# Kernel optimization log

Measured on AMD Instinct MI355X. Metric: run time of the kernel, lower is better.

## Reference

```python
import jax, jax.numpy as jnp
import numpy as np

B, LQ, LK = 4, 2048, 2048
DQ, DK, DO = 1024, 1024, 1024


def setup_inputs() -> dict:
    key = jax.random.key(0)
    ks = jax.random.split(key, 9)
    s = 0.02
    return {
        "query_input": jax.random.normal(ks[0], (B, LQ, DQ), jnp.float32),
        "key_input": jax.random.normal(ks[1], (B, LK, DK), jnp.float32),
        "value_input": jax.random.normal(ks[2], (B, LK, DK), jnp.float32),
        "Wq": jax.random.normal(ks[3], (DQ, DO), jnp.float32) * s,
        "bq": jax.random.normal(ks[4], (DO,), jnp.float32) * s,
        "Wk": jax.random.normal(ks[5], (DK, DO), jnp.float32) * s,
        "bk": jax.random.normal(ks[6], (DO,), jnp.float32) * s,
        "Wv": jax.random.normal(ks[7], (DK, DO), jnp.float32) * s,
        "bv": jax.random.normal(ks[8], (DO,), jnp.float32) * s,
    }


def reference(query_input, key_input, value_input, Wq, bq, Wk, bk, Wv, bv):
    scale = jnp.asarray(DO, query_input.dtype) ** 0.5
    q = query_input @ Wq + bq              # [B, Lq, D]
    k = key_input @ Wk + bk                # [B, Lk, D]
    v = value_input @ Wv + bv              # [B, Lk, D]
    attn = jnp.einsum("bqd,bkd->bqk", q, k) / scale
    attn = jax.nn.softmax(attn, axis=-1)
    return jnp.einsum("bqk,bkd->bqd", attn, v)
```

## Files before the change

kernel.cpp:

```cpp
#include <hip/hip_runtime.h>

typedef _Float16 f16x8 __attribute__((ext_vector_type(8)));
typedef _Float16 f16x4 __attribute__((ext_vector_type(4)));
typedef float f32x4 __attribute__((ext_vector_type(4)));

__device__ __forceinline__ void lds_load16(const _Float16* g, _Float16* l) {
    __builtin_amdgcn_global_load_lds(
        (const __attribute__((address_space(1))) void*)g,
        (__attribute__((address_space(3))) void*)l,
        16, 0, 0);
}

template <int BIAS_MODE, bool OUT_F32>
__global__ __launch_bounds__(256, 2)
void gemm_nt_f16(const _Float16* __restrict__ A, const _Float16* __restrict__ B,
                 void* __restrict__ Cv, const float* __restrict__ bias,
                 int M, int N, int K, int lda, int ldb, int ldc,
                 long long strideA, long long strideB, long long strideC,
                 float alpha)
{
    const int z = blockIdx.z;
    A += (size_t)z * strideA;
    B += (size_t)z * strideB;

    const int m0 = blockIdx.y * 128;
    const int n0 = blockIdx.x * 128;

    __shared__ __align__(16) _Float16 As[128 * 32];
    __shared__ __align__(16) _Float16 Bs[128 * 32];

    const int t    = threadIdx.x;
    const int w    = t >> 6;
    const int lane = t & 63;
    const int ln   = lane & 15;
    const int kq   = lane >> 4;
    const int wm   = (w & 1) * 64;
    const int wn   = (w >> 1) * 64;

    const int arow = t >> 2;
    const int kc   = (t & 3) * 8;
    const _Float16* gA0 = A + (size_t)(m0 + arow) * lda + kc;
    const _Float16* gA1 = A + (size_t)(m0 + 64 + arow) * lda + kc;
    const _Float16* gB0 = B + (size_t)(n0 + arow) * ldb + kc;
    const _Float16* gB1 = B + (size_t)(n0 + 64 + arow) * ldb + kc;
    _Float16* lA0 = As + w * 512;
    _Float16* lA1 = As + 2048 + w * 512;
    _Float16* lB0 = Bs + w * 512;
    _Float16* lB1 = Bs + 2048 + w * 512;

    f32x4 acc[4][4] = {};

    for (int k0 = 0; k0 < K; k0 += 32) {
        __syncthreads();
        lds_load16(gA0 + k0, lA0);
        lds_load16(gA1 + k0, lA1);
        lds_load16(gB0 + k0, lB0);
        lds_load16(gB1 + k0, lB1);
        __syncthreads();

        f16x8 af[4], bf[4];
#pragma unroll
        for (int i = 0; i < 4; ++i)
            af[i] = *(const f16x8*)(As + (wm + i * 16 + ln) * 32 + kq * 8);
#pragma unroll
        for (int i = 0; i < 4; ++i)
            bf[i] = *(const f16x8*)(Bs + (wn + i * 16 + ln) * 32 + kq * 8);
#pragma unroll
        for (int i = 0; i < 4; ++i)
#pragma unroll
            for (int j = 0; j < 4; ++j)
                acc[i][j] = __builtin_amdgcn_mfma_f32_16x16x32_f16(af[i], bf[j], acc[i][j], 0, 0, 0);
    }

    float*     Cf = (float*)Cv;
    _Float16*  Ch = (_Float16*)Cv;
    const size_t cbase = (size_t)z * strideC;
#pragma unroll
    for (int i = 0; i < 4; ++i) {
        const int rbase = m0 + wm + i * 16 + kq * 4;
#pragma unroll
        for (int j = 0; j < 4; ++j) {
            const int gcol = n0 + wn + j * 16 + ln;
#pragma unroll
            for (int r = 0; r < 4; ++r) {
                float vv = acc[i][j][r] * alpha;
                if (BIAS_MODE == 1) vv += bias[gcol];
                if (BIAS_MODE == 2) vv += bias[rbase + r];
                const size_t idx = cbase + (size_t)(rbase + r) * ldc + gcol;
                if (OUT_F32) Cf[idx] = vv;
                else         Ch[idx] = (_Float16)vv;
            }
        }
    }
}

__global__ __launch_bounds__(256)
void cvt_f32_f16(const float4* __restrict__ x, _Float16* __restrict__ y)
{
    const size_t i = (size_t)blockIdx.x * 256 + threadIdx.x;
    float4 f = x[i];
    f16x4 o = { (_Float16)f.x, (_Float16)f.y, (_Float16)f.z, (_Float16)f.w };
    *(f16x4*)(y + i * 4) = o;
}

__global__ __launch_bounds__(256)
void transpose_w_1024(const float* __restrict__ W, _Float16* __restrict__ WT)
{
    __shared__ float tile[32][33];
    const int bx = blockIdx.x * 32;
    const int by = blockIdx.y * 32;
    const int tx = threadIdx.x;
    const int ty = threadIdx.y;
#pragma unroll
    for (int i = ty; i < 32; i += 8)
        tile[i][tx] = W[(size_t)(by + i) * 1024 + bx + tx];
    __syncthreads();
#pragma unroll
    for (int i = ty; i < 32; i += 8)
        WT[(size_t)(bx + i) * 1024 + by + tx] = (_Float16)tile[tx][i];
}

__global__ __launch_bounds__(256)
void softmax_rows_2048(_Float16* __restrict__ S)
{
    const size_t row = blockIdx.x;
    _Float16* p = S + row * 2048;
    const int t = threadIdx.x, lane = t & 63, w = t >> 6;

    f16x8 v = *(const f16x8*)(p + t * 8);
    float x[8];
    float mx = -3.4e38f;
#pragma unroll
    for (int i = 0; i < 8; ++i) { x[i] = (float)v[i]; mx = fmaxf(mx, x[i]); }
#pragma unroll
    for (int off = 32; off > 0; off >>= 1) mx = fmaxf(mx, __shfl_xor(mx, off));

    __shared__ float rmax[4], rsum[4];
    if (lane == 0) rmax[w] = mx;
    __syncthreads();
    mx = fmaxf(fmaxf(rmax[0], rmax[1]), fmaxf(rmax[2], rmax[3]));

    float s = 0.f;
#pragma unroll
    for (int i = 0; i < 8; ++i) { x[i] = __expf(x[i] - mx); s += x[i]; }
#pragma unroll
    for (int off = 32; off > 0; off >>= 1) s += __shfl_xor(s, off);
    if (lane == 0) rsum[w] = s;
    __syncthreads();
    s = rsum[0] + rsum[1] + rsum[2] + rsum[3];

    const float inv = 1.f / s;
    f16x8 o;
#pragma unroll
    for (int i = 0; i < 8; ++i) o[i] = (_Float16)(x[i] * inv);
    *(f16x8*)(p + t * 8) = o;
}

extern "C" void kernel_launch(void* const* d_in, const int* in_sizes, int n_in,
                              void* d_out, int out_size, void* d_ws, size_t ws_size,
                              hipStream_t stream)
{
    const float* Xq = (const float*)d_in[0];
    const float* Xk = (const float*)d_in[1];
    const float* Xv = (const float*)d_in[2];
    const float* Wq = (const float*)d_in[3];
    const float* bq = (const float*)d_in[4];
    const float* Wk = (const float*)d_in[5];
    const float* bk = (const float*)d_in[6];
    const float* Wv = (const float*)d_in[7];
    const float* bv = (const float*)d_in[8];
    float* out = (float*)d_out;

    const size_t XN = (size_t)8192 * 1024;
    const size_t WN = (size_t)1024 * 1024;

    _Float16* ws  = (_Float16*)d_ws;
    _Float16* Xqh = ws;
    _Float16* Xkh = Xqh + XN;
    _Float16* Xvh = Xkh + XN;
    _Float16* WqT = Xvh + XN;
    _Float16* WkT = WqT + WN;
    _Float16* WvT = WkT + WN;
    _Float16* qh  = WvT + WN;
    _Float16* kh  = qh + XN;
    _Float16* vT  = kh + XN;
    _Float16* S   = vT + XN;

    cvt_f32_f16<<<8192, 256, 0, stream>>>((const float4*)Xq, Xqh);
    cvt_f32_f16<<<8192, 256, 0, stream>>>((const float4*)Xk, Xkh);
    cvt_f32_f16<<<8192, 256, 0, stream>>>((const float4*)Xv, Xvh);

    {
        dim3 tb(32, 8), tg(32, 32);
        transpose_w_1024<<<tg, tb, 0, stream>>>(Wq, WqT);
        transpose_w_1024<<<tg, tb, 0, stream>>>(Wk, WkT);
        transpose_w_1024<<<tg, tb, 0, stream>>>(Wv, WvT);
    }

    {
        dim3 g(1024 / 128, 8192 / 128, 1);
        gemm_nt_f16<1, false><<<g, 256, 0, stream>>>(Xqh, WqT, qh, bq,
            8192, 1024, 1024, 1024, 1024, 1024, 0, 0, 0, 1.f);
        gemm_nt_f16<1, false><<<g, 256, 0, stream>>>(Xkh, WkT, kh, bk,
            8192, 1024, 1024, 1024, 1024, 1024, 0, 0, 0, 1.f);
    }
    {
        dim3 g(8192 / 128, 1024 / 128, 1);
        gemm_nt_f16<2, false><<<g, 256, 0, stream>>>(WvT, Xvh, vT, bv,
            1024, 8192, 1024, 1024, 1024, 8192, 0, 0, 0, 1.f);
    }

    {
        dim3 g(2048 / 128, 2048 / 128, 4);
        gemm_nt_f16<0, false><<<g, 256, 0, stream>>>(qh, kh, S, nullptr,
            2048, 2048, 1024, 1024, 1024, 2048,
            (long long)2048 * 1024, (long long)2048 * 1024, (long long)2048 * 2048,
            0.03125f);
    }

    softmax_rows_2048<<<8192, 256, 0, stream>>>(S);

    {
        dim3 g(1024 / 128, 2048 / 128, 4);
        gemm_nt_f16<0, true><<<g, 256, 0, stream>>>(S, vT, out, nullptr,
            2048, 1024, 2048, 2048, 8192, 1024,
            (long long)2048 * 2048, (long long)2048, (long long)2048 * 1024,
            1.f);
    }
}
```

Measured before the change: 369.6 us.

## Fuse softmax into QK and PV GEMM epilogues and batch small launches

The standalone softmax kernel is removed. The QK^T GEMM now writes exp(score) in fp16 and atomically accumulates row sums, with no max subtraction. The PV GEMM splits K into two halves, scales by the inverse row sum and accumulates into a zeroed output with float atomics. The three input conversions, the three weight transposes and the Q/K projections are each merged into one launch to cut launch overhead. Dropping the max subtraction risks overflow for larger logits, and split-K atomics make the summation order nondeterministic.

```diff
diff --git a/kernel.cpp b/kernel.cpp
--- a/kernel.cpp
+++ b/kernel.cpp
@@ -11,17 +11,30 @@
         16, 0, 0);
 }
 
-template <int BIAS_MODE, bool OUT_F32>
+template <int MODE>
 __global__ __launch_bounds__(256, 2)
-void gemm_nt_f16(const _Float16* __restrict__ A, const _Float16* __restrict__ B,
-                 void* __restrict__ Cv, const float* __restrict__ bias,
-                 int M, int N, int K, int lda, int ldb, int ldc,
-                 long long strideA, long long strideB, long long strideC,
-                 float alpha)
+void gemm_nt(const _Float16* A, const _Float16* B, void* Cv, const float* bias,
+             const _Float16* A2, const _Float16* B2, const float* bias2, void* C2,
+             float* rowsum,
+             int M, int N, int K, int lda, int ldb, int ldc,
+             long long strideA, long long strideB, long long strideC, float alpha)
 {
     const int z = blockIdx.z;
-    A += (size_t)z * strideA;
-    B += (size_t)z * strideB;
+    size_t cbase = 0;
+    if (MODE == 1) {
+        if (z) { A = A2; B = B2; bias = bias2; Cv = C2; }
+    } else if (MODE == 3) {
+        A += (size_t)z * strideA;
+        B += (size_t)z * strideB;
+        cbase = (size_t)z * strideC;
+        rowsum += (size_t)z * M;
+    } else if (MODE == 4) {
+        const int b = z >> 1, kc = z & 1;
+        A += (size_t)b * strideA + (size_t)kc * 1024;
+        B += (size_t)b * 2048 + (size_t)kc * 1024;
+        cbase = (size_t)b * strideC;
+        rowsum += (size_t)b * M;
+    }
 
     const int m0 = blockIdx.y * 128;
     const int n0 = blockIdx.x * 128;
@@ -38,11 +51,11 @@
     const int wn   = (w >> 1) * 64;
 
     const int arow = t >> 2;
-    const int kc   = (t & 3) * 8;
-    const _Float16* gA0 = A + (size_t)(m0 + arow) * lda + kc;
-    const _Float16* gA1 = A + (size_t)(m0 + 64 + arow) * lda + kc;
-    const _Float16* gB0 = B + (size_t)(n0 + arow) * ldb + kc;
-    const _Float16* gB1 = B + (size_t)(n0 + 64 + arow) * ldb + kc;
+    const int kcf  = (t & 3) * 8;
+    const _Float16* gA0 = A + (size_t)(m0 + arow) * lda + kcf;
+    const _Float16* gA1 = A + (size_t)(m0 + 64 + arow) * lda + kcf;
+    const _Float16* gB0 = B + (size_t)(n0 + arow) * ldb + kcf;
+    const _Float16* gB1 = B + (size_t)(n0 + 64 + arow) * ldb + kcf;
     _Float16* lA0 = As + w * 512;
     _Float16* lA1 = As + 2048 + w * 512;
     _Float16* lB0 = Bs + w * 512;
@@ -72,40 +85,86 @@
                 acc[i][j] = __builtin_amdgcn_mfma_f32_16x16x32_f16(af[i], bf[j], acc[i][j], 0, 0, 0);
     }
 
-    float*     Cf = (float*)Cv;
-    _Float16*  Ch = (_Float16*)Cv;
-    const size_t cbase = (size_t)z * strideC;
+    float*    Cf = (float*)Cv;
+    _Float16* Ch = (_Float16*)Cv;
 #pragma unroll
     for (int i = 0; i < 4; ++i) {
         const int rbase = m0 + wm + i * 16 + kq * 4;
-#pragma unroll
-        for (int j = 0; j < 4; ++j) {
-            const int gcol = n0 + wn + j * 16 + ln;
+
+        if (MODE == 1 || MODE == 2) {
+#pragma unroll
+            for (int j = 0; j < 4; ++j) {
+                const int gcol = n0 + wn + j * 16 + ln;
+#pragma unroll
+                for (int r = 0; r < 4; ++r) {
+                    float vv = acc[i][j][r];
+                    if (MODE == 1) vv += bias[gcol];
+                    if (MODE == 2) vv += bias[rbase + r];
+                    Ch[cbase + (size_t)(rbase + r) * ldc + gcol] = (_Float16)vv;
+                }
+            }
+        } else if (MODE == 3) {
+            float rs[4] = {0.f, 0.f, 0.f, 0.f};
+#pragma unroll
+            for (int j = 0; j < 4; ++j) {
+                const int gcol = n0 + wn + j * 16 + ln;
+#pragma unroll
+                for (int r = 0; r < 4; ++r) {
+                    float e = __expf(acc[i][j][r] * alpha);
+                    Ch[cbase + (size_t)(rbase + r) * ldc + gcol] = (_Float16)e;
+                    rs[r] += e;
+                }
+            }
 #pragma unroll
             for (int r = 0; r < 4; ++r) {
-                float vv = acc[i][j][r] * alpha;
-                if (BIAS_MODE == 1) vv += bias[gcol];
-                if (BIAS_MODE == 2) vv += bias[rbase + r];
-                const size_t idx = cbase + (size_t)(rbase + r) * ldc + gcol;
-                if (OUT_F32) Cf[idx] = vv;
-                else         Ch[idx] = (_Float16)vv;
+                float s = rs[r];
+                s += __shfl_xor(s, 1);
+                s += __shfl_xor(s, 2);
+                s += __shfl_xor(s, 4);
+                s += __shfl_xor(s, 8);
+                if (ln == 0) atomicAdd(&rowsum[rbase + r], s);
+            }
+        } else if (MODE == 4) {
+            float inv[4];
+#pragma unroll
+            for (int r = 0; r < 4; ++r) inv[r] = 1.f / rowsum[rbase + r];
+#pragma unroll
+            for (int j = 0; j < 4; ++j) {
+                const int gcol = n0 + wn + j * 16 + ln;
+#pragma unroll
+                for (int r = 0; r < 4; ++r)
+                    atomicAdd(&Cf[cbase + (size_t)(rbase + r) * ldc + gcol],
+                              acc[i][j][r] * inv[r]);
             }
         }
     }
 }
 
 __global__ __launch_bounds__(256)
-void cvt_f32_f16(const float4* __restrict__ x, _Float16* __restrict__ y)
+void cvt_and_zero(const float4* __restrict__ x0, _Float16* __restrict__ y0,
+                  const float4* __restrict__ x1, _Float16* __restrict__ y1,
+                  const float4* __restrict__ x2, _Float16* __restrict__ y2,
+                  float* __restrict__ rowsum, float4* __restrict__ outz)
 {
     const size_t i = (size_t)blockIdx.x * 256 + threadIdx.x;
+    const float4* x = blockIdx.y == 0 ? x0 : blockIdx.y == 1 ? x1 : x2;
+    _Float16*    yy = blockIdx.y == 0 ? y0 : blockIdx.y == 1 ? y1 : y2;
     float4 f = x[i];
     f16x4 o = { (_Float16)f.x, (_Float16)f.y, (_Float16)f.z, (_Float16)f.w };
-    *(f16x4*)(y + i * 4) = o;
+    *(f16x4*)(yy + i * 4) = o;
+    if (blockIdx.y == 0 && blockIdx.x < 32)
+        rowsum[blockIdx.x * 256 + threadIdx.x] = 0.f;
+    if (blockIdx.y == 1)
+        outz[i] = make_float4(0.f, 0.f, 0.f, 0.f);
 }
 
 __global__ __launch_bounds__(256)
-void transpose_w_1024(const float* __restrict__ W, _Float16* __restrict__ WT)
-{
+void transpose_w_1024(const float* __restrict__ W0, _Float16* __restrict__ T0,
+                      const float* __restrict__ W1, _Float16* __restrict__ T1,
+                      const float* __restrict__ W2, _Float16* __restrict__ T2)
+{
+    const float* W = blockIdx.z == 0 ? W0 : blockIdx.z == 1 ? W1 : W2;
+    _Float16*   WT = blockIdx.z == 0 ? T0 : blockIdx.z == 1 ? T1 : T2;
     __shared__ float tile[32][33];
     const int bx = blockIdx.x * 32;
     const int by = blockIdx.y * 32;
@@ -118,42 +177,6 @@
 #pragma unroll
     for (int i = ty; i < 32; i += 8)
         WT[(size_t)(bx + i) * 1024 + by + tx] = (_Float16)tile[tx][i];
-}
-
-__global__ __launch_bounds__(256)
-void softmax_rows_2048(_Float16* __restrict__ S)
-{
-    const size_t row = blockIdx.x;
-    _Float16* p = S + row * 2048;
-    const int t = threadIdx.x, lane = t & 63, w = t >> 6;
-
-    f16x8 v = *(const f16x8*)(p + t * 8);
-    float x[8];
-    float mx = -3.4e38f;
-#pragma unroll
-    for (int i = 0; i < 8; ++i) { x[i] = (float)v[i]; mx = fmaxf(mx, x[i]); }
-#pragma unroll
-    for (int off = 32; off > 0; off >>= 1) mx = fmaxf(mx, __shfl_xor(mx, off));
-
-    __shared__ float rmax[4], rsum[4];
-    if (lane == 0) rmax[w] = mx;
-    __syncthreads();
-    mx = fmaxf(fmaxf(rmax[0], rmax[1]), fmaxf(rmax[2], rmax[3]));
-
-    float s = 0.f;
-#pragma unroll
-    for (int i = 0; i < 8; ++i) { x[i] = __expf(x[i] - mx); s += x[i]; }
-#pragma unroll
-    for (int off = 32; off > 0; off >>= 1) s += __shfl_xor(s, off);
-    if (lane == 0) rsum[w] = s;
-    __syncthreads();
-    s = rsum[0] + rsum[1] + rsum[2] + rsum[3];
-
-    const float inv = 1.f / s;
-    f16x8 o;
-#pragma unroll
-    for (int i = 0; i < 8; ++i) o[i] = (_Float16)(x[i] * inv);
-    *(f16x8*)(p + t * 8) = o;
 }
 
 extern "C" void kernel_launch(void* const* d_in, const int* in_sizes, int n_in,
@@ -185,46 +208,49 @@
     _Float16* kh  = qh + XN;
     _Float16* vT  = kh + XN;
     _Float16* S   = vT + XN;
-
-    cvt_f32_f16<<<8192, 256, 0, stream>>>((const float4*)Xq, Xqh);
-    cvt_f32_f16<<<8192, 256, 0, stream>>>((const float4*)Xk, Xkh);
-    cvt_f32_f16<<<8192, 256, 0, stream>>>((const float4*)Xv, Xvh);
-
-    {
-        dim3 tb(32, 8), tg(32, 32);
-        transpose_w_1024<<<tg, tb, 0, stream>>>(Wq, WqT);
-        transpose_w_1024<<<tg, tb, 0, stream>>>(Wk, WkT);
-        transpose_w_1024<<<tg, tb, 0, stream>>>(Wv, WvT);
-    }
-
-    {
-        dim3 g(1024 / 128, 8192 / 128, 1);
-        gemm_nt_f16<1, false><<<g, 256, 0, stream>>>(Xqh, WqT, qh, bq,
+    float* rowsum = (float*)(S + (size_t)4 * 2048 * 2048);
+
+    {
+        dim3 g(8192, 3);
+        cvt_and_zero<<<g, 256, 0, stream>>>((const float4*)Xq, Xqh,
+                                            (const float4*)Xk, Xkh,
+                                            (const float4*)Xv, Xvh,
+                                            rowsum, (float4*)out);
+    }
+
+    {
+        dim3 tb(32, 8), tg(32, 32, 3);
+        transpose_w_1024<<<tg, tb, 0, stream>>>(Wq, WqT, Wk, WkT, Wv, WvT);
+    }
+
+    {
+        dim3 g(8, 64, 2);
+        gemm_nt<1><<<g, 256, 0, stream>>>(Xqh, WqT, qh, bq,
+            Xkh, WkT, bk, kh, nullptr,
             8192, 1024, 1024, 1024, 1024, 1024, 0, 0, 0, 1.f);
-        gemm_nt_f16<1, false><<<g, 256, 0, stream>>>(Xkh, WkT, kh, bk,
-            8192, 1024, 1024, 1024, 1024, 1024, 0, 0, 0, 1.f);
-    }
-    {
-        dim3 g(8192 / 128, 1024 / 128, 1);
-        gemm_nt_f16<2, false><<<g, 256, 0, stream>>>(WvT, Xvh, vT, bv,
+    }
+    {
+        dim3 g(64, 8, 1);
+        gemm_nt<2><<<g, 256, 0, stream>>>(WvT, Xvh, vT, bv,
+            nullptr, nullptr, nullptr, nullptr, nullptr,
             1024, 8192, 1024, 1024, 1024, 8192, 0, 0, 0, 1.f);
     }
 
     {
-        dim3 g(2048 / 128, 2048 / 128, 4);
-        gemm_nt_f16<0, false><<<g, 256, 0, stream>>>(qh, kh, S, nullptr,
+        dim3 g(16, 16, 4);
+        gemm_nt<3><<<g, 256, 0, stream>>>(qh, kh, S, nullptr,
+            nullptr, nullptr, nullptr, nullptr, rowsum,
             2048, 2048, 1024, 1024, 1024, 2048,
             (long long)2048 * 1024, (long long)2048 * 1024, (long long)2048 * 2048,
             0.03125f);
     }
 
-    softmax_rows_2048<<<8192, 256, 0, stream>>>(S);
-
-    {
-        dim3 g(1024 / 128, 2048 / 128, 4);
-        gemm_nt_f16<0, true><<<g, 256, 0, stream>>>(S, vT, out, nullptr,
-            2048, 1024, 2048, 2048, 8192, 1024,
-            (long long)2048 * 2048, (long long)2048, (long long)2048 * 1024,
+    {
+        dim3 g(8, 16, 8);
+        gemm_nt<4><<<g, 256, 0, stream>>>(S, vT, out, nullptr,
+            nullptr, nullptr, nullptr, nullptr, rowsum,
+            2048, 1024, 1024, 2048, 8192, 1024,
+            (long long)2048 * 2048, 0, (long long)2048 * 1024,
             1.f);
     }
 }
```

Measured after the change: 371.7 us. Within noise of the previous version (+0.6%).
